# Kernel optimization log

Hardware: AMD Instinct MI355X
Metric: run time of the kernel (lower is better)

The kernel has to match this reference:

```python
import jax, jax.numpy as jnp
import numpy as np


def setup_inputs() -> dict:
    key = jax.random.key(0)
    k1, k2, k3, k4, k5 = jax.random.split(key, 5)
    B, N, C = 16, 1024, 768
    x = jax.random.normal(k1, (B, N, C), dtype=jnp.float32)
    sc_token = jax.random.normal(k2, (1, 196, C), dtype=jnp.float32) * 0.02  # trunc_normal std=0.02
    W_qkv = jax.random.normal(k3, (C, 3 * C), dtype=jnp.float32) * 0.02
    W_proj = jax.random.normal(k4, (C, C), dtype=jnp.float32) * 0.02
    b_proj = jax.random.normal(k5, (C,), dtype=jnp.float32) * 0.02
    return {"x": x, "sc_token": sc_token, "W_qkv": W_qkv, "W_proj": W_proj, "b_proj": b_proj}


def reference(x, sc_token, W_qkv, W_proj, b_proj):
    B, N, C = x.shape
    H = 12
    Dh = C // H
    scale = Dh ** -0.5
    # concat learnable style/content tokens: [B, N1, C]
    xt = jnp.concatenate([x, jnp.broadcast_to(sc_token, (B,) + sc_token.shape[1:])], axis=1)
    N1 = xt.shape[1]
    qkv = (xt @ W_qkv).reshape(B, N1, 3, H, Dh)
    q = qkv[:, :, 0].transpose(0, 2, 1, 3)  # [B,H,N1,Dh]
    k = qkv[:, :, 1].transpose(0, 2, 1, 3)
    v = qkv[:, :, 2].transpose(0, 2, 1, 3)
    attn = jax.nn.softmax(jnp.einsum('bhqd,bhkd->bhqk', q, k) * scale, axis=-1)
    out = jnp.einsum('bhqk,bhkd->bhqd', attn, v)  # [B,H,N1,Dh]
    out = out.transpose(0, 2, 1, 3).reshape(B, N1, C)
    out = out[:, :N, :]  # drop appended tokens
    return out @ W_proj + b_proj
```

## Files before the change

### kernel.cpp

```cpp
#include <hip/hip_runtime.h>
#include <hip/hip_bf16.h>

#define BB 16
#define NN 1024
#define CC 768
#define HH 12
#define DH 64
#define NSC 196
#define N1 1220
#define MPAD 19584
#define M_QKV (BB * N1)
#define N_QKV (3 * CC)
#define M_PROJ (BB * NN)
#define KP 1224

typedef __attribute__((ext_vector_type(8))) short short8;
typedef __attribute__((ext_vector_type(4))) float f32x4;

#define SC2F 0.18033688011f

__device__ __forceinline__ void load_lds16(const void* g, void* l) {
    __builtin_amdgcn_global_load_lds(
        (__attribute__((address_space(1))) void*)(g),
        (__attribute__((address_space(3))) void*)(l),
        16, 0, 0);
}

__global__ __launch_bounds__(256) void cast_xt_kernel(
    const float* __restrict__ x, const float* __restrict__ sct,
    __hip_bfloat16* __restrict__ xt)
{
    const int e   = blockIdx.x * 256 + threadIdx.x;
    const int row = e / 96;
    const int c8  = (e - row * 96) * 8;
    union { short8 s; __hip_bfloat16 h[8]; } u;
    if (row < M_QKV) {
        const int b  = row / N1;
        const int rr = row - b * N1;
        const float* src = (rr < NN)
            ? x   + ((size_t)b * NN + rr) * CC + c8
            : sct + (size_t)(rr - NN) * CC + c8;
        const float4 v0 = *(const float4*)src;
        const float4 v1 = *(const float4*)(src + 4);
        u.h[0] = __float2bfloat16(v0.x); u.h[1] = __float2bfloat16(v0.y);
        u.h[2] = __float2bfloat16(v0.z); u.h[3] = __float2bfloat16(v0.w);
        u.h[4] = __float2bfloat16(v1.x); u.h[5] = __float2bfloat16(v1.y);
        u.h[6] = __float2bfloat16(v1.z); u.h[7] = __float2bfloat16(v1.w);
    } else {
#pragma unroll
        for (int j = 0; j < 8; ++j) u.h[j] = __float2bfloat16(0.f);
    }
    *(short8*)(xt + (size_t)row * CC + c8) = u.s;
}

__global__ __launch_bounds__(256) void cast_wt_kernel(
    const float* __restrict__ W, __hip_bfloat16* __restrict__ WT, int Ncols)
{
    const int e  = blockIdx.x * 256 + threadIdx.x;
    const int n  = e / 96;
    const int k8 = (e - n * 96) * 8;
    union { short8 s; __hip_bfloat16 h[8]; } u;
#pragma unroll
    for (int j = 0; j < 8; ++j)
        u.h[j] = __float2bfloat16(W[(size_t)(k8 + j) * Ncols + n]);
    *(short8*)(WT + (size_t)n * CC + k8) = u.s;
}

__global__ __launch_bounds__(256) void transpose_v_kernel(
    const __hip_bfloat16* __restrict__ qkv, __hip_bfloat16* __restrict__ vt)
{
    __shared__ short Ls[64 * 72];
    const int t  = threadIdx.x;
    const int kt = blockIdx.x, h = blockIdx.y, b = blockIdx.z;
    const __hip_bfloat16* vb = qkv + (size_t)b * N1 * N_QKV + 2 * CC + h * DH;

#pragma unroll
    for (int i = 0; i < 2; ++i) {
        const int c   = t + 256 * i;
        const int key = c >> 3;
        const int d8  = (c & 7) * 8;
        const int kg  = kt * 64 + key;
        union { short8 s; short hh[8]; } u;
        if (kg < N1) {
            u.s = *(const short8*)(vb + (size_t)kg * N_QKV + d8);
        } else {
#pragma unroll
            for (int j = 0; j < 8; ++j) u.hh[j] = 0;
        }
#pragma unroll
        for (int j = 0; j < 8; ++j) Ls[(d8 + j) * 72 + key] = u.hh[j];
    }
    __syncthreads();
    __hip_bfloat16* ob = vt + (size_t)(b * HH + h) * 64 * KP + kt * 64;
#pragma unroll
    for (int i = 0; i < 2; ++i) {
        const int c  = t + 256 * i;
        const int d  = c >> 3;
        const int k8 = (c & 7) * 8;
        if (kt * 64 + k8 < KP)
            *(short8*)(ob + (size_t)d * KP + k8) = *(const short8*)&Ls[d * 72 + k8];
    }
}

template <bool WRITE_BF16, bool QSCALE>
__global__ __launch_bounds__(256) void mfma_gemm_bt(
    const __hip_bfloat16* __restrict__ A,
    const __hip_bfloat16* __restrict__ BT,
    void* __restrict__ Cout,
    const float* __restrict__ bias,
    int lda, int K, int ldc)
{
    __shared__ __hip_bfloat16 As[128 * 32];
    __shared__ __hip_bfloat16 Bs[128 * 32];

    const int t    = threadIdx.x;
    const int lane = t & 63;
    const int l15  = lane & 15;
    const int quad = lane >> 4;
    const int w    = t >> 6;
    const int wm   = w & 1;
    const int wn   = w >> 1;

    const int nwg = gridDim.x * gridDim.y;
    const int lin = blockIdx.y * gridDim.x + blockIdx.x;
    const int qq  = nwg >> 3, rr = nwg & 7;
    const int xcd = lin & 7, off = lin >> 3;
    const int sw  = ((xcd < rr) ? xcd * (qq + 1)
                                : rr * (qq + 1) + (xcd - rr) * qq) + off;
    const int n0 = (sw % gridDim.x) * 128;
    const int m0 = (sw / gridDim.x) * 128;

    const int f0 = t * 16;
    const int r0 = f0 >> 6, c0 = (f0 & 63) >> 1;
    const int r1 = (f0 + 4096) >> 6, c1 = c0;

    const __hip_bfloat16* gA0 = A  + (size_t)(m0 + r0) * lda + c0;
    const __hip_bfloat16* gA1 = A  + (size_t)(m0 + r1) * lda + c1;
    const __hip_bfloat16* gB0 = BT + (size_t)(n0 + r0) * K + c0;
    const __hip_bfloat16* gB1 = BT + (size_t)(n0 + r1) * K + c1;

    __hip_bfloat16* lA0 = As + r0 * 32 + c0;
    __hip_bfloat16* lA1 = As + r1 * 32 + c1;
    __hip_bfloat16* lB0 = Bs + r0 * 32 + c0;
    __hip_bfloat16* lB1 = Bs + r1 * 32 + c1;

    f32x4 acc[4][4];
#pragma unroll
    for (int mi = 0; mi < 4; ++mi)
#pragma unroll
        for (int ni = 0; ni < 4; ++ni) {
            acc[mi][ni][0] = 0.f; acc[mi][ni][1] = 0.f;
            acc[mi][ni][2] = 0.f; acc[mi][ni][3] = 0.f;
        }

    for (int k0 = 0; k0 < K; k0 += 32) {
        __syncthreads();
        load_lds16(gA0, lA0);
        load_lds16(gA1, lA1);
        load_lds16(gB0, lB0);
        load_lds16(gB1, lB1);
        gA0 += 32; gA1 += 32; gB0 += 32; gB1 += 32;
        __syncthreads();

        short8 af[4], bf_[4];
#pragma unroll
        for (int mi = 0; mi < 4; ++mi)
            af[mi] = *(const short8*)&As[(wm * 64 + mi * 16 + l15) * 32 + quad * 8];
#pragma unroll
        for (int ni = 0; ni < 4; ++ni)
            bf_[ni] = *(const short8*)&Bs[(wn * 64 + ni * 16 + l15) * 32 + quad * 8];
#pragma unroll
        for (int mi = 0; mi < 4; ++mi)
#pragma unroll
            for (int ni = 0; ni < 4; ++ni)
                acc[mi][ni] = __builtin_amdgcn_mfma_f32_16x16x32_bf16(
                    af[mi], bf_[ni], acc[mi][ni], 0, 0, 0);
    }

#pragma unroll
    for (int mi = 0; mi < 4; ++mi) {
        const int rowb = m0 + wm * 64 + mi * 16 + quad * 4;
#pragma unroll
        for (int ni = 0; ni < 4; ++ni) {
            const int col = n0 + wn * 64 + ni * 16 + l15;
#pragma unroll
            for (int r = 0; r < 4; ++r) {
                const size_t idx = (size_t)(rowb + r) * ldc + col;
                if (WRITE_BF16) {
                    float v = acc[mi][ni][r];
                    if (QSCALE && n0 < CC) v *= SC2F;
                    ((__hip_bfloat16*)Cout)[idx] = __float2bfloat16(v);
                } else {
                    ((float*)Cout)[idx] = acc[mi][ni][r] + bias[col];
                }
            }
        }
    }
}

__global__ __launch_bounds__(256, 4) void attn_mfma_kernel(
    const __hip_bfloat16* qkv,
    const __hip_bfloat16* __restrict__ vt,
    __hip_bfloat16* ao)
{
    __shared__ __hip_bfloat16 Ks[64 * 64];
    __shared__ __hip_bfloat16 Vs[64 * 64];
    __shared__ short Pl[4 * 16 * 64];

    const int t    = threadIdx.x;
    const int l15  = t & 15;
    const int quad = (t >> 4) & 3;
    const int w    = t >> 6;
    const int swz  = l15 & 7;

    const int L    = blockIdx.x + 16 * (blockIdx.y + 12 * blockIdx.z);
    const int g    = L & 7, s = L >> 3;
    const int pair = g * 24 + (s >> 4);
    const int qt   = s & 15;
    const int h    = pair % 12;
    const int b    = pair / 12;

    const size_t rowbase = (size_t)b * N1;
    const __hip_bfloat16* qb  = qkv + rowbase * N_QKV + h * DH;
    const __hip_bfloat16* kb  = qkv + rowbase * N_QKV + CC + h * DH;
    const __hip_bfloat16* vtb = vt + (size_t)(b * HH + h) * 64 * KP;

    const int cA = t,       rA = cA >> 3, uA = (cA & 7) ^ (rA & 7);
    const int cB = t + 256, rB = cB >> 3, uB = (cB & 7) ^ (rB & 7);

    short8 qf[2];
    {
        const size_t qrow = (size_t)(qt * 64 + w * 16 + l15);
#pragma unroll
        for (int ks = 0; ks < 2; ++ks)
            qf[ks] = *(const short8*)(qb + qrow * N_QKV + ks * 32 + quad * 8);
    }

    f32x4 oac[4];
#pragma unroll
    for (int dt = 0; dt < 4; ++dt) {
        oac[dt][0] = 0.f; oac[dt][1] = 0.f; oac[dt][2] = 0.f; oac[dt][3] = 0.f;
    }
    float lrun = 0.f;
    short* Pw = Pl + (w * 16) * 64;

    for (int k0 = 0; k0 < N1; k0 += 64) {
        __syncthreads();
        load_lds16(kb  + (size_t)(k0 + rA) * N_QKV + uA * 8, (char*)Ks + cA * 16);
        load_lds16(kb  + (size_t)(k0 + rB) * N_QKV + uB * 8, (char*)Ks + cB * 16);
        load_lds16(vtb + (size_t)rA * KP + k0 + uA * 8,      (char*)Vs + cA * 16);
        load_lds16(vtb + (size_t)rB * KP + k0 + uB * 8,      (char*)Vs + cB * 16);
        __syncthreads();

        short8 kf[4][2];
#pragma unroll
        for (int mt = 0; mt < 4; ++mt)
#pragma unroll
            for (int ks = 0; ks < 2; ++ks)
                kf[mt][ks] = *(const short8*)
                    &Ks[(mt * 16 + l15) * 64 + ((4 * ks + quad) ^ swz) * 8];

        f32x4 st[4];
#pragma unroll
        for (int mt = 0; mt < 4; ++mt) {
            st[mt][0] = 0.f; st[mt][1] = 0.f; st[mt][2] = 0.f; st[mt][3] = 0.f;
        }
        __builtin_amdgcn_s_setprio(1);
#pragma unroll
        for (int ks = 0; ks < 2; ++ks)
#pragma unroll
            for (int mt = 0; mt < 4; ++mt)
                st[mt] = __builtin_amdgcn_mfma_f32_16x16x32_bf16(
                    kf[mt][ks], qf[ks], st[mt], 0, 0, 0);
        __builtin_amdgcn_s_setprio(0);

        if (k0 + 64 > N1) {
#pragma unroll
            for (int mt = 0; mt < 4; ++mt)
#pragma unroll
                for (int r = 0; r < 4; ++r)
                    if (k0 + mt * 16 + quad * 4 + r >= N1) st[mt][r] = -1e30f;
        }
        float rsum = 0.f;
#pragma unroll
        for (int mt = 0; mt < 4; ++mt)
#pragma unroll
            for (int r = 0; r < 4; ++r) {
                const float p = exp2f(st[mt][r]);
                st[mt][r] = p;
                rsum += p;
            }
        rsum += __shfl_xor(rsum, 16);
        rsum += __shfl_xor(rsum, 32);
        lrun += rsum;

#pragma unroll
        for (int mt = 0; mt < 4; ++mt) {
            union { unsigned long long u; __hip_bfloat16 hh[4]; } pk;
#pragma unroll
            for (int r = 0; r < 4; ++r) pk.hh[r] = __float2bfloat16(st[mt][r]);
            const int unit = (2 * mt + (quad >> 1)) ^ swz;
            *(unsigned long long*)&Pw[l15 * 64 + unit * 8 + (quad & 1) * 4] = pk.u;
        }

        __builtin_amdgcn_s_setprio(1);
#pragma unroll
        for (int ks = 0; ks < 2; ++ks) {
            const short8 pf = *(const short8*)
                &Pw[l15 * 64 + ((4 * ks + quad) ^ swz) * 8];
#pragma unroll
            for (int dt = 0; dt < 4; ++dt) {
                const short8 vf = *(const short8*)
                    &Vs[(l15 + 16 * dt) * 64 + ((4 * ks + quad) ^ swz) * 8];
                oac[dt] = __builtin_amdgcn_mfma_f32_16x16x32_bf16(pf, vf, oac[dt], 0, 0, 0);
            }
        }
        __builtin_amdgcn_s_setprio(0);
    }

    const float li = 1.0f / lrun;
#pragma unroll
    for (int r = 0; r < 4; ++r) {
        const float ir = __shfl(li, quad * 4 + r);
        const int qrow = qt * 64 + w * 16 + quad * 4 + r;
        __hip_bfloat16* orow = ao + ((size_t)b * NN + qrow) * N_QKV + h * DH;
#pragma unroll
        for (int dt = 0; dt < 4; ++dt)
            orow[l15 + 16 * dt] = __float2bfloat16(oac[dt][r] * ir);
    }
}

extern "C" void kernel_launch(void* const* d_in, const int* in_sizes, int n_in,
                              void* d_out, int out_size, void* d_ws, size_t ws_size,
                              hipStream_t stream) {
    const float* x      = (const float*)d_in[0];
    const float* sct    = (const float*)d_in[1];
    const float* W_qkv  = (const float*)d_in[2];
    const float* W_proj = (const float*)d_in[3];
    const float* b_proj = (const float*)d_in[4];
    float* out = (float*)d_out;

    char* p = (char*)d_ws;
    __hip_bfloat16* xt      = (__hip_bfloat16*)p;
    __hip_bfloat16* vtg     = (__hip_bfloat16*)p;
    __hip_bfloat16* qkv     = (__hip_bfloat16*)(p + (size_t)MPAD * CC * 2);
    __hip_bfloat16* WTqkv   = (__hip_bfloat16*)(p + (size_t)MPAD * CC * 2 + (size_t)MPAD * N_QKV * 2);
    __hip_bfloat16* WTproj  = WTqkv + (size_t)N_QKV * CC;
    __hip_bfloat16* ao      = qkv + 2 * CC;

    cast_xt_kernel<<<MPAD * 96 / 256, 256, 0, stream>>>(x, sct, xt);
    cast_wt_kernel<<<N_QKV * 96 / 256, 256, 0, stream>>>(W_qkv, WTqkv, N_QKV);
    cast_wt_kernel<<<CC * 96 / 256, 256, 0, stream>>>(W_proj, WTproj, CC);

    mfma_gemm_bt<true, true><<<dim3(N_QKV / 128, MPAD / 128), 256, 0, stream>>>(
        xt, WTqkv, qkv, nullptr, CC, CC, N_QKV);
    transpose_v_kernel<<<dim3((N1 + 63) / 64, HH, BB), 256, 0, stream>>>(qkv, vtg);
    attn_mfma_kernel<<<dim3(NN / 64, HH, BB), 256, 0, stream>>>(qkv, vtg, ao);
    mfma_gemm_bt<false, false><<<dim3(CC / 128, M_PROJ / 128), 256, 0, stream>>>(
        ao, WTproj, out, b_proj, N_QKV, CC, CC);
}
```

Before: 379.8 us.

## Prefetch next K/V tile in attention and deepen GEMM K-step with swizzled LDS

The attention kernel now issues loads for the next K tile and a double-buffered V tile right after the QK^T MFMAs, so the global-to-LDS traffic overlaps with softmax and the PV matmul instead of stalling at the start of each iteration. The GEMM doubles its K-tile from 32 to 64, halving the number of barriers per output tile, and stores the LDS tiles with an XOR swizzle to avoid bank conflicts. Both raise LDS use per block, which may lower occupancy. The attention loop also still has two barriers per iteration.

```diff
diff --git a/kernel.cpp b/kernel.cpp
--- a/kernel.cpp
+++ b/kernel.cpp
@@ -110,8 +110,8 @@
     const float* __restrict__ bias,
     int lda, int K, int ldc)
 {
-    __shared__ __hip_bfloat16 As[128 * 32];
-    __shared__ __hip_bfloat16 Bs[128 * 32];
+    __shared__ __hip_bfloat16 As[128 * 64];
+    __shared__ __hip_bfloat16 Bs[128 * 64];
 
     const int t    = threadIdx.x;
     const int lane = t & 63;
@@ -120,6 +120,7 @@
     const int w    = t >> 6;
     const int wm   = w & 1;
     const int wn   = w >> 1;
+    const int swz  = l15 & 7;
 
     const int nwg = gridDim.x * gridDim.y;
     const int lin = blockIdx.y * gridDim.x + blockIdx.x;
@@ -130,19 +131,13 @@
     const int n0 = (sw % gridDim.x) * 128;
     const int m0 = (sw / gridDim.x) * 128;
 
-    const int f0 = t * 16;
-    const int r0 = f0 >> 6, c0 = (f0 & 63) >> 1;
-    const int r1 = (f0 + 4096) >> 6, c1 = c0;
-
-    const __hip_bfloat16* gA0 = A  + (size_t)(m0 + r0) * lda + c0;
-    const __hip_bfloat16* gA1 = A  + (size_t)(m0 + r1) * lda + c1;
-    const __hip_bfloat16* gB0 = BT + (size_t)(n0 + r0) * K + c0;
-    const __hip_bfloat16* gB1 = BT + (size_t)(n0 + r1) * K + c1;
-
-    __hip_bfloat16* lA0 = As + r0 * 32 + c0;
-    __hip_bfloat16* lA1 = As + r1 * 32 + c1;
-    __hip_bfloat16* lB0 = Bs + r0 * 32 + c0;
-    __hip_bfloat16* lB1 = Bs + r1 * 32 + c1;
+    const int rr0 = t >> 3;
+    const int uu  = ((t & 7) ^ (rr0 & 7)) * 8;
+
+    const __hip_bfloat16* gA = A  + (size_t)(m0 + rr0) * lda + uu;
+    const __hip_bfloat16* gB = BT + (size_t)(n0 + rr0) * K   + uu;
+    __hip_bfloat16* lA = As + t * 8;
+    __hip_bfloat16* lB = Bs + t * 8;
 
     f32x4 acc[4][4];
 #pragma unroll
@@ -153,28 +148,36 @@
             acc[mi][ni][2] = 0.f; acc[mi][ni][3] = 0.f;
         }
 
-    for (int k0 = 0; k0 < K; k0 += 32) {
+    for (int k0 = 0; k0 < K; k0 += 64) {
         __syncthreads();
-        load_lds16(gA0, lA0);
-        load_lds16(gA1, lA1);
-        load_lds16(gB0, lB0);
-        load_lds16(gB1, lB1);
-        gA0 += 32; gA1 += 32; gB0 += 32; gB1 += 32;
+        load_lds16(gA,            lA);
+        load_lds16(gA + 32 * lda, lA + 2048);
+        load_lds16(gA + 64 * lda, lA + 4096);
+        load_lds16(gA + 96 * lda, lA + 6144);
+        load_lds16(gB,            lB);
+        load_lds16(gB + 32 * K,   lB + 2048);
+        load_lds16(gB + 64 * K,   lB + 4096);
+        load_lds16(gB + 96 * K,   lB + 6144);
+        gA += 64; gB += 64;
         __syncthreads();
 
-        short8 af[4], bf_[4];
-#pragma unroll
-        for (int mi = 0; mi < 4; ++mi)
-            af[mi] = *(const short8*)&As[(wm * 64 + mi * 16 + l15) * 32 + quad * 8];
-#pragma unroll
-        for (int ni = 0; ni < 4; ++ni)
-            bf_[ni] = *(const short8*)&Bs[(wn * 64 + ni * 16 + l15) * 32 + quad * 8];
-#pragma unroll
-        for (int mi = 0; mi < 4; ++mi)
+#pragma unroll
+        for (int ks = 0; ks < 2; ++ks) {
+            short8 af[4], bf_[4];
+            const int u = ((ks * 4 + quad) ^ swz) * 8;
+#pragma unroll
+            for (int mi = 0; mi < 4; ++mi)
+                af[mi] = *(const short8*)&As[(wm * 64 + mi * 16 + l15) * 64 + u];
 #pragma unroll
             for (int ni = 0; ni < 4; ++ni)
-                acc[mi][ni] = __builtin_amdgcn_mfma_f32_16x16x32_bf16(
-                    af[mi], bf_[ni], acc[mi][ni], 0, 0, 0);
+                bf_[ni] = *(const short8*)&Bs[(wn * 64 + ni * 16 + l15) * 64 + u];
+#pragma unroll
+            for (int mi = 0; mi < 4; ++mi)
+#pragma unroll
+                for (int ni = 0; ni < 4; ++ni)
+                    acc[mi][ni] = __builtin_amdgcn_mfma_f32_16x16x32_bf16(
+                        af[mi], bf_[ni], acc[mi][ni], 0, 0, 0);
+        }
     }
 
 #pragma unroll
@@ -204,7 +207,7 @@
     __hip_bfloat16* ao)
 {
     __shared__ __hip_bfloat16 Ks[64 * 64];
-    __shared__ __hip_bfloat16 Vs[64 * 64];
+    __shared__ __hip_bfloat16 Vs[2][64 * 64];
     __shared__ short Pl[4 * 16 * 64];
 
     const int t    = threadIdx.x;
@@ -228,6 +231,15 @@
     const int cA = t,       rA = cA >> 3, uA = (cA & 7) ^ (rA & 7);
     const int cB = t + 256, rB = cB >> 3, uB = (cB & 7) ^ (rB & 7);
 
+#define KSTAGE(k0) do {                                                            \
+        load_lds16(kb + (size_t)((k0) + rA) * N_QKV + uA * 8, (char*)Ks + cA * 16); \
+        load_lds16(kb + (size_t)((k0) + rB) * N_QKV + uB * 8, (char*)Ks + cB * 16); \
+    } while (0)
+#define VSTAGE(bi, k0) do {                                                        \
+        load_lds16(vtb + (size_t)rA * KP + (k0) + uA * 8, (char*)&Vs[(bi)][0] + cA * 16); \
+        load_lds16(vtb + (size_t)rB * KP + (k0) + uB * 8, (char*)&Vs[(bi)][0] + cB * 16); \
+    } while (0)
+
     short8 qf[2];
     {
         const size_t qrow = (size_t)(qt * 64 + w * 16 + l15);
@@ -244,14 +256,12 @@
     float lrun = 0.f;
     short* Pw = Pl + (w * 16) * 64;
 
+    KSTAGE(0);
+    VSTAGE(0, 0);
+    __syncthreads();
+
+    int cur = 0;
     for (int k0 = 0; k0 < N1; k0 += 64) {
-        __syncthreads();
-        load_lds16(kb  + (size_t)(k0 + rA) * N_QKV + uA * 8, (char*)Ks + cA * 16);
-        load_lds16(kb  + (size_t)(k0 + rB) * N_QKV + uB * 8, (char*)Ks + cB * 16);
-        load_lds16(vtb + (size_t)rA * KP + k0 + uA * 8,      (char*)Vs + cA * 16);
-        load_lds16(vtb + (size_t)rB * KP + k0 + uB * 8,      (char*)Vs + cB * 16);
-        __syncthreads();
-
         short8 kf[4][2];
 #pragma unroll
         for (int mt = 0; mt < 4; ++mt)
@@ -273,6 +283,13 @@
                 st[mt] = __builtin_amdgcn_mfma_f32_16x16x32_bf16(
                     kf[mt][ks], qf[ks], st[mt], 0, 0, 0);
         __builtin_amdgcn_s_setprio(0);
+
+        __syncthreads();
+
+        if (k0 + 64 < N1) {
+            KSTAGE(k0 + 64);
+            VSTAGE(cur ^ 1, k0 + 64);
+        }
 
         if (k0 + 64 > N1) {
 #pragma unroll
@@ -311,12 +328,17 @@
 #pragma unroll
             for (int dt = 0; dt < 4; ++dt) {
                 const short8 vf = *(const short8*)
-                    &Vs[(l15 + 16 * dt) * 64 + ((4 * ks + quad) ^ swz) * 8];
+                    &Vs[cur][(l15 + 16 * dt) * 64 + ((4 * ks + quad) ^ swz) * 8];
                 oac[dt] = __builtin_amdgcn_mfma_f32_16x16x32_bf16(pf, vf, oac[dt], 0, 0, 0);
             }
         }
         __builtin_amdgcn_s_setprio(0);
-    }
+
+        __syncthreads();
+        cur ^= 1;
+    }
+#undef KSTAGE
+#undef VSTAGE
 
     const float li = 1.0f / lrun;
 #pragma unroll
```

New measurement: 347.3 us. -8.6%, faster.
